# Kernel tuning notes

Hardware: AMD Instinct MI355X
Metric: run time of the kernel (lower is better)

## Reference

```python
import jax, jax.numpy as jnp
import numpy as np

N_NODES = 50000   # number of graph nodes
N_EDGES = 800000  # avg degree 16
D = 128           # in_dim == all hdims -> residual active every layer
L = 3             # len(cfg['hdims'])


def setup_inputs() -> dict:
    key = jax.random.key(0)
    ks = jax.random.split(key, 8)
    scale = 1.0 / np.sqrt(D)
    x = jax.random.normal(ks[0], (N_NODES, D), dtype=jnp.float32)
    edge_index = jax.random.randint(ks[1], (2, N_EDGES), 0, N_NODES, dtype=jnp.int32)
    in_fc_w = jax.random.normal(ks[2], (D, D), dtype=jnp.float32) * scale
    in_fc_b = jnp.zeros((D,), dtype=jnp.float32)
    # GraphConv per layer: lin_rel (with bias) applied to aggregated neighbors,
    # lin_root (no bias) applied to self features. All layers are DxD -> stack.
    w_rel = jax.random.normal(ks[3], (L, D, D), dtype=jnp.float32) * scale
    b_rel = jnp.zeros((L, D), dtype=jnp.float32)
    w_root = jax.random.normal(ks[4], (L, D, D), dtype=jnp.float32) * scale
    return {"x": x, "edge_index": edge_index, "in_fc_w": in_fc_w,
            "in_fc_b": in_fc_b, "w_rel": w_rel, "b_rel": b_rel, "w_root": w_root}


def reference(x, edge_index, in_fc_w, in_fc_b, w_rel, b_rel, w_root):
    src, dst = edge_index[0], edge_index[1]
    h = x @ in_fc_w + in_fc_b                     # in_fc
    for l in range(L):                            # fixed small layer count
        # GraphConv, aggr='add': gather source feats, scatter-add to targets
        agg = jax.ops.segment_sum(h[src], dst, num_segments=N_NODES)  # [N, D]
        out = agg @ w_rel[l] + b_rel[l] + h @ w_root[l]
        out = jax.nn.relu(out)
        h = out + h                               # residual (dims match)
    return h
```

## Files before the change

kernel.cpp:

```cpp
#include <hip/hip_runtime.h>
#include <hip/hip_bf16.h>


constexpr int D = 128;
constexpr int NB_SHIFT = 7;
constexpr int BCAP = 2560;
constexpr int STRIDE = 3456;
constexpr int CHUNK = 2048;
constexpr int NRANGE = 16;

typedef __attribute__((ext_vector_type(8))) short bf16x8;
typedef __attribute__((ext_vector_type(4))) float f32x4;
typedef __attribute__((ext_vector_type(4))) unsigned int u32x4;

__device__ inline unsigned short f2bf(float f) {
    unsigned int u = __builtin_bit_cast(unsigned int, f);
    u += 0x7FFFu + ((u >> 16) & 1u);
    return (unsigned short)(u >> 16);
}
__device__ inline float bf2f(unsigned short v) {
    return __builtin_bit_cast(float, (unsigned int)v << 16);
}
__device__ inline float bf2f_lo(unsigned int v) {
    return __builtin_bit_cast(float, v << 16);
}
__device__ inline float bf2f_hi(unsigned int v) {
    return __builtin_bit_cast(float, v & 0xFFFF0000u);
}

__global__ __launch_bounds__(256) void prep(
    const float* __restrict__ fc_w, const float* __restrict__ w_rel,
    const float* __restrict__ w_root, unsigned short* __restrict__ Wp,
    int* __restrict__ cursor, unsigned short* __restrict__ hb0,
    unsigned short* __restrict__ hb1, int NB, int N)
{
    int blk = blockIdx.x;
    if (blk < 56) {
        int idx = blk * 256 + threadIdx.x;
        int mat  = idx >> 11;
        int rem  = idx & 2047;
        int tn   = rem >> 8;
        int ks   = (rem >> 6) & 3;
        int lane = rem & 63;
        const float* w = (mat == 0) ? fc_w
                       : (mat <= 3) ? w_rel  + (size_t)(mat - 1) * D * D
                                    : w_root + (size_t)(mat - 4) * D * D;
        unsigned short* wp = Wp + (size_t)mat * D * D + (size_t)rem * 8;
        int kbase = ks * 32 + (lane >> 4) * 8;
        int col   = tn * 16 + (lane & 15);
        #pragma unroll
        for (int j = 0; j < 8; ++j)
            wp[j] = f2bf(w[(size_t)(kbase + j) * D + col]);
        return;
    }
    blk -= 56;
    const int ncb = (NB + 255) / 256;
    if (blk < ncb) {
        int i = blk * 256 + threadIdx.x;
        if (i < NB) cursor[i] = 0;
        return;
    }
    if (threadIdx.x < 64)
        ((unsigned int*)(hb0 + (size_t)N * D))[threadIdx.x] = 0u;
    else if (threadIdx.x < 128)
        ((unsigned int*)(hb1 + (size_t)N * D))[threadIdx.x - 64] = 0u;
}

__global__ __launch_bounds__(256) void scatter_gemm(
    const int* __restrict__ src, const int* __restrict__ dst,
    unsigned int* __restrict__ entries, int* __restrict__ cursor, int E, int NB, int NS,
    const float* __restrict__ x, const unsigned short* __restrict__ W1p,
    const float* __restrict__ bias, unsigned short* __restrict__ hb_out, int N)
{
    const int tid = threadIdx.x;

    if (blockIdx.x < (unsigned)NS) {
        __shared__ unsigned int   stage[CHUNK];
        __shared__ unsigned short bslot[CHUNK];
        __shared__ int lhist[512];
        __shared__ int lscan[512];
        __shared__ int lgbase[512];
        __shared__ int lcur[512];
        __shared__ int sh[256];

        const int base  = blockIdx.x * CHUNK;
        const int count = min(CHUNK, E - base);

        for (int i = tid; i < 512; i += 256) { lhist[i] = 0; lcur[i] = 0; }
        __syncthreads();

        for (int i = tid; i < count; i += 256)
            atomicAdd(&lhist[dst[base + i] >> NB_SHIFT], 1);
        __syncthreads();

        int v2 = lhist[2 * tid] + lhist[2 * tid + 1];
        sh[tid] = v2;
        __syncthreads();
        #pragma unroll
        for (int off = 1; off < 256; off <<= 1) {
            int t = (tid >= off) ? sh[tid - off] : 0;
            __syncthreads();
            sh[tid] += t;
            __syncthreads();
        }
        int excl2 = sh[tid] - v2;
        lscan[2 * tid]     = excl2;
        lscan[2 * tid + 1] = excl2 + lhist[2 * tid];
        __syncthreads();

        for (int t = tid; t < 512; t += 256) {
            int c = (t < NB) ? lhist[t] : 0;
            lgbase[t] = (c > 0) ? atomicAdd(&cursor[t], c) : 0;
        }
        __syncthreads();

        for (int i = tid; i < count; i += 256) {
            int d = dst[base + i];
            int s = src[base + i];
            int b = d >> NB_SHIFT;
            int p = atomicAdd(&lcur[b], 1);
            int slot = lscan[b] + p;
            stage[slot] = ((unsigned int)(d & ((1 << NB_SHIFT) - 1)) << 16) | (unsigned int)s;
            bslot[slot] = (unsigned short)b;
        }
        __syncthreads();

        for (int i = tid; i < count; i += 256) {
            int b   = bslot[i];
            int off = i - lscan[b] + lgbase[b];
            if (off < BCAP) entries[(size_t)b * BCAP + off] = stage[i];
        }
        return;
    }

    const int blk  = blockIdx.x - NS;
    const int wave = tid >> 6;
    const int lane = tid & 63;
    const int row0 = blk * 64 + wave * 16;
    const int mrow = lane & 15;
    const int kgrp = lane >> 4;

    f32x4 acc[8];
    #pragma unroll
    for (int t = 0; t < 8; ++t) acc[t] = (f32x4){0.f, 0.f, 0.f, 0.f};

    int arow = row0 + mrow; if (arow >= N) arow = N - 1;
    const float* xr = x + (size_t)arow * D + kgrp * 8;

    #pragma unroll
    for (int ks = 0; ks < 4; ++ks) {
        float4 f0 = *(const float4*)(xr + ks * 32);
        float4 f1 = *(const float4*)(xr + ks * 32 + 4);
        bf16x8 a1;
        a1[0] = (short)f2bf(f0.x); a1[1] = (short)f2bf(f0.y);
        a1[2] = (short)f2bf(f0.z); a1[3] = (short)f2bf(f0.w);
        a1[4] = (short)f2bf(f1.x); a1[5] = (short)f2bf(f1.y);
        a1[6] = (short)f2bf(f1.z); a1[7] = (short)f2bf(f1.w);
        #pragma unroll
        for (int tn = 0; tn < 8; ++tn) {
            bf16x8 b = *(const bf16x8*)(W1p + ((size_t)((tn * 4 + ks) * 64 + lane) * 8));
            acc[tn] = __builtin_amdgcn_mfma_f32_16x16x32_bf16(a1, b, acc[tn], 0, 0, 0);
        }
    }

    const int r0 = row0 + kgrp * 4;
    #pragma unroll
    for (int tn = 0; tn < 8; ++tn) {
        const int col = tn * 16 + mrow;
        const float bv = bias[col];
        #pragma unroll
        for (int reg = 0; reg < 4; ++reg) {
            int r = r0 + reg;
            if (r < N) hb_out[(size_t)r * D + col] = f2bf(acc[tn][reg] + bv);
        }
    }
}

__global__ __launch_bounds__(256) void bucket_sort(
    const unsigned int* __restrict__ entries, const int* __restrict__ cursor,
    unsigned int* __restrict__ sorted_off, int* __restrict__ eb,
    int N, int NB, float inv_range, unsigned int zero_off)
{
    const int b   = blockIdx.x;
    const int tid = threadIdx.x;

    __shared__ int nhist[128 * NRANGE];
    __shared__ int nscan[128 * NRANGE];
    __shared__ int ncur[128 * NRANGE];
    __shared__ int nbase[129];
    __shared__ int sh[256];
    __shared__ unsigned int svals[STRIDE];

    const int cnt = min(cursor[b], BCAP);

    for (int i = tid; i < 128 * NRANGE; i += 256) { nhist[i] = 0; ncur[i] = 0; }
    __syncthreads();

    const unsigned int* ebase = entries + (size_t)b * BCAP;
    for (int i = tid; i < cnt; i += 256) {
        unsigned int e = ebase[i];
        int s = (int)(e & 0xFFFFu);
        int r = (int)((float)s * inv_range); if (r > NRANGE - 1) r = NRANGE - 1;
        atomicAdd(&nhist[(int)((e >> 16) << 4) | r], 1);
    }
    __syncthreads();

    int c4 = 0, pc = 0;
    if (tid < 128) {
        int s = 0;
        #pragma unroll
        for (int q = 0; q < NRANGE; ++q) s += nhist[NRANGE * tid + q];
        c4 = s;
        pc = (c4 + 7) & ~7;
    }
    sh[tid] = (tid < 128) ? pc : 0;
    __syncthreads();
    #pragma unroll
    for (int off = 1; off < 128; off <<= 1) {
        int t = (tid >= off && tid < 128) ? sh[tid - off] : 0;
        __syncthreads();
        if (tid < 128) sh[tid] += t;
        __syncthreads();
    }
    if (tid < 128) nbase[tid] = sh[tid] - pc;
    if (tid == 127) nbase[128] = sh[127];
    __syncthreads();
    const int padded_total = nbase[128];

    if (tid < 128) {
        int base = nbase[tid];
        int run = base;
        #pragma unroll
        for (int q = 0; q < NRANGE; ++q) {
            nscan[NRANGE * tid + q] = run;
            run += nhist[NRANGE * tid + q];
        }
        int nn = (b << NB_SHIFT) + tid;
        if (nn < N) {
            eb[2 * nn]     = b * STRIDE + base;
            eb[2 * nn + 1] = b * STRIDE + base + pc;
        }
    }
    for (int i = tid; i < padded_total; i += 256) svals[i] = zero_off;
    __syncthreads();

    for (int i = tid; i < cnt; i += 256) {
        unsigned int e = ebase[i];
        int s = (int)(e & 0xFFFFu);
        int r = (int)((float)s * inv_range); if (r > NRANGE - 1) r = NRANGE - 1;
        int key = (int)((e >> 16) << 4) | r;
        int p = atomicAdd(&ncur[key], 1);
        svals[nscan[key] + p] = ((unsigned int)s) << 8;
    }
    __syncthreads();

    unsigned int* obase = sorted_off + (size_t)b * STRIDE;
    for (int i = tid; i < padded_total; i += 256) obase[i] = svals[i];
}

__global__ __launch_bounds__(256) void layer_fused(
    const unsigned short* __restrict__ hb_in, const int* __restrict__ eb,
    const unsigned int* __restrict__ sorted_off,
    const unsigned short* __restrict__ Wrel, const unsigned short* __restrict__ Wroot,
    const float* __restrict__ bias,
    unsigned short* hb_out, float* out_f32, int N)
{
    __shared__ unsigned short aggt[16][136];

    const int tid   = threadIdx.x;
    const int wave  = tid >> 6;
    const int lane  = tid & 63;
    const int node0 = blockIdx.x * 16;

    {
        const int g = lane >> 4;
        const int c = lane & 15;
        const int n = node0 + wave * 4 + g;

        float acc[8];
        #pragma unroll
        for (int q = 0; q < 8; ++q) acc[q] = 0.f;

        if (n < N) {
            const int2 be = ((const int2*)eb)[n];
            int j = be.x;
            const int e = be.y;
            const unsigned int c16 = (unsigned int)c * 16u;
            const char* hb = (const char*)hb_in;
            if (j < e) {
                u32x4 iA = *(const u32x4*)(sorted_off + j);
                u32x4 iB = *(const u32x4*)(sorted_off + j + 4);
                for (;;) {
                    u32x4 v0 = *(const u32x4*)(hb + (iA[0] + c16));
                    u32x4 v1 = *(const u32x4*)(hb + (iA[1] + c16));
                    u32x4 v2 = *(const u32x4*)(hb + (iA[2] + c16));
                    u32x4 v3 = *(const u32x4*)(hb + (iA[3] + c16));
                    u32x4 v4 = *(const u32x4*)(hb + (iB[0] + c16));
                    u32x4 v5 = *(const u32x4*)(hb + (iB[1] + c16));
                    u32x4 v6 = *(const u32x4*)(hb + (iB[2] + c16));
                    u32x4 v7 = *(const u32x4*)(hb + (iB[3] + c16));
                    const bool more = (j + 8 < e);
                    u32x4 nA, nB;
                    if (more) {
                        nA = *(const u32x4*)(sorted_off + j + 8);
                        nB = *(const u32x4*)(sorted_off + j + 12);
                    }
                    #pragma unroll
                    for (int q = 0; q < 4; ++q) {
                        acc[2 * q]     += ((bf2f_lo(v0[q]) + bf2f_lo(v1[q])) + (bf2f_lo(v2[q]) + bf2f_lo(v3[q])))
                                        + ((bf2f_lo(v4[q]) + bf2f_lo(v5[q])) + (bf2f_lo(v6[q]) + bf2f_lo(v7[q])));
                        acc[2 * q + 1] += ((bf2f_hi(v0[q]) + bf2f_hi(v1[q])) + (bf2f_hi(v2[q]) + bf2f_hi(v3[q])))
                                        + ((bf2f_hi(v4[q]) + bf2f_hi(v5[q])) + (bf2f_hi(v6[q]) + bf2f_hi(v7[q])));
                    }
                    if (!more) break;
                    iA = nA; iB = nB; j += 8;
                }
            }
        }
        u32x4 o;
        #pragma unroll
        for (int q = 0; q < 4; ++q)
            o[q] = (unsigned int)f2bf(acc[2 * q]) |
                   ((unsigned int)f2bf(acc[2 * q + 1]) << 16);
        *(u32x4*)&aggt[wave * 4 + g][c * 8] = o;
    }
    __syncthreads();

    const int mrow = lane & 15;
    const int kgrp = lane >> 4;

    f32x4 acc2[2];
    acc2[0] = (f32x4){0.f, 0.f, 0.f, 0.f};
    acc2[1] = (f32x4){0.f, 0.f, 0.f, 0.f};

    int arow = node0 + mrow; if (arow >= N) arow = N - 1;
    const size_t abase = (size_t)arow * D + kgrp * 8;

    #pragma unroll
    for (int ks = 0; ks < 4; ++ks) {
        bf16x8 a1 = *(const bf16x8*)&aggt[mrow][ks * 32 + kgrp * 8];
        bf16x8 a2 = *(const bf16x8*)(hb_in + abase + ks * 32);
        #pragma unroll
        for (int t = 0; t < 2; ++t) {
            const int tn = wave * 2 + t;
            bf16x8 b1 = *(const bf16x8*)(Wrel  + ((size_t)((tn * 4 + ks) * 64 + lane) * 8));
            acc2[t] = __builtin_amdgcn_mfma_f32_16x16x32_bf16(a1, b1, acc2[t], 0, 0, 0);
            bf16x8 b2 = *(const bf16x8*)(Wroot + ((size_t)((tn * 4 + ks) * 64 + lane) * 8));
            acc2[t] = __builtin_amdgcn_mfma_f32_16x16x32_bf16(a2, b2, acc2[t], 0, 0, 0);
        }
    }

    const int r0 = node0 + kgrp * 4;
    #pragma unroll
    for (int t = 0; t < 2; ++t) {
        const int tn  = wave * 2 + t;
        const int col = tn * 16 + mrow;
        const float bv = bias[col];
        #pragma unroll
        for (int reg = 0; reg < 4; ++reg) {
            int r = r0 + reg;
            if (r < N) {
                float z = fmaxf(acc2[t][reg] + bv, 0.f);
                float o = z + bf2f(hb_in[(size_t)r * D + col]);
                if (out_f32 != nullptr) out_f32[(size_t)r * D + col] = o;
                else                    hb_out[(size_t)r * D + col] = f2bf(o);
            }
        }
    }
}

extern "C" void kernel_launch(void* const* d_in, const int* in_sizes, int n_in,
                              void* d_out, int out_size, void* d_ws, size_t ws_size,
                              hipStream_t stream)
{
    const float* x      = (const float*)d_in[0];
    const int*   ei     = (const int*)  d_in[1];
    const float* fc_w   = (const float*)d_in[2];
    const float* fc_b   = (const float*)d_in[3];
    const float* w_rel  = (const float*)d_in[4];
    const float* b_rel  = (const float*)d_in[5];
    const float* w_root = (const float*)d_in[6];
    float* out = (float*)d_out;

    const int N = in_sizes[0] / D;
    const int E = in_sizes[1] / 2;
    const int* src = ei;
    const int* dst = ei + E;
    const int NB = (N + (1 << NB_SHIFT) - 1) >> NB_SHIFT;

    char* p = (char*)d_ws;
    unsigned short* hb0 = (unsigned short*)p;  p += (size_t)(N + 1) * D * sizeof(unsigned short);
    unsigned short* hb1 = (unsigned short*)p;  p += (size_t)(N + 1) * D * sizeof(unsigned short);
    unsigned short* Wp  = (unsigned short*)p;  p += (size_t)7 * D * D * sizeof(unsigned short);
    unsigned int* sorted_off = (unsigned int*)p;  p += (size_t)NB * STRIDE * sizeof(unsigned int);
    int* eb     = (int*)p;                     p += (size_t)2 * N * sizeof(int);
    int* cursor = (int*)p;                     p += (size_t)NB * sizeof(int);
    unsigned int* entries = (unsigned int*)d_out;

    unsigned short* Wp_in   = Wp;
    unsigned short* Wp_rel  = Wp + (size_t)1 * D * D;
    unsigned short* Wp_root = Wp + (size_t)4 * D * D;

    const int NS = (E + CHUNK - 1) / CHUNK;
    const int gemm_blocks  = (N + 63) / 64;
    const int layer_blocks = (N + 15) / 16;
    const int prep_blocks  = 56 + (NB + 255) / 256 + 1;

    prep<<<prep_blocks, 256, 0, stream>>>(fc_w, w_rel, w_root, Wp, cursor,
                                          hb0, hb1, NB, N);

    scatter_gemm<<<NS + gemm_blocks, 256, 0, stream>>>(
        src, dst, entries, cursor, E, NB, NS,
        x, Wp_in, fc_b, hb0, N);

    bucket_sort<<<NB, 256, 0, stream>>>(
        entries, cursor, sorted_off, eb, N, NB, (float)NRANGE / (float)N,
        ((unsigned int)N) << 8);

    unsigned short* hin  = hb0;
    unsigned short* hout = hb1;
    for (int l = 0; l < 3; ++l) {
        layer_fused<<<layer_blocks, 256, 0, stream>>>(
            hin, eb, sorted_off,
            Wp_rel + (size_t)l * D * D, Wp_root + (size_t)l * D * D,
            b_rel + (size_t)l * D,
            (l == 2) ? nullptr : hout,
            (l == 2) ? out : nullptr, N);
        unsigned short* t = hin; hin = hout; hout = t;
    }
}
```

Measured before the change: 229.5 us.

## Split node features into column chunks and separate gather from GEMM

Stores the bf16 node features as four column chunks of 32 features each, so a gather block only touches a 3.2 MB slice that fits in cache better. Each layer is split into a chunk-parallel gather kernel that writes the aggregate to global memory, plus a separate GEMM/epilogue kernel. Sorted source indices are compressed from 32-bit byte offsets to 16-bit node ids. This adds an extra round trip through global memory for the aggregate and one more launch per layer. The 16-bit ids only hold while N is below 65536.

New measurement: 247.5 us. 1.08x slower.

```diff
diff --git a/kernel.cpp b/kernel.cpp
--- a/kernel.cpp
+++ b/kernel.cpp
@@ -32,7 +32,7 @@
     const float* __restrict__ fc_w, const float* __restrict__ w_rel,
     const float* __restrict__ w_root, unsigned short* __restrict__ Wp,
     int* __restrict__ cursor, unsigned short* __restrict__ hb0,
-    unsigned short* __restrict__ hb1, int NB, int N)
+    unsigned short* __restrict__ hb1, int NB, int N, int CSr)
 {
     int blk = blockIdx.x;
     if (blk < 56) {
@@ -60,17 +60,22 @@
         if (i < NB) cursor[i] = 0;
         return;
     }
-    if (threadIdx.x < 64)
-        ((unsigned int*)(hb0 + (size_t)N * D))[threadIdx.x] = 0u;
-    else if (threadIdx.x < 128)
-        ((unsigned int*)(hb1 + (size_t)N * D))[threadIdx.x - 64] = 0u;
+    const int t = threadIdx.x;
+    if (t < 64) {
+        int c = t >> 4, w = t & 15;
+        ((unsigned int*)(hb0 + (size_t)c * CSr + (size_t)N * 32))[w] = 0u;
+    } else if (t < 128) {
+        int tt = t - 64;
+        int c = tt >> 4, w = tt & 15;
+        ((unsigned int*)(hb1 + (size_t)c * CSr + (size_t)N * 32))[w] = 0u;
+    }
 }
 
 __global__ __launch_bounds__(256) void scatter_gemm(
     const int* __restrict__ src, const int* __restrict__ dst,
     unsigned int* __restrict__ entries, int* __restrict__ cursor, int E, int NB, int NS,
     const float* __restrict__ x, const unsigned short* __restrict__ W1p,
-    const float* __restrict__ bias, unsigned short* __restrict__ hb_out, int N)
+    const float* __restrict__ bias, unsigned short* __restrict__ hb_out, int N, int CSr)
 {
     const int tid = threadIdx.x;
 
@@ -168,18 +173,21 @@
     for (int tn = 0; tn < 8; ++tn) {
         const int col = tn * 16 + mrow;
         const float bv = bias[col];
+        const int c  = col >> 5;
+        const int cc = col & 31;
         #pragma unroll
         for (int reg = 0; reg < 4; ++reg) {
             int r = r0 + reg;
-            if (r < N) hb_out[(size_t)r * D + col] = f2bf(acc[tn][reg] + bv);
+            if (r < N)
+                hb_out[(size_t)c * CSr + (size_t)r * 32 + cc] = f2bf(acc[tn][reg] + bv);
         }
     }
 }
 
 __global__ __launch_bounds__(256) void bucket_sort(
     const unsigned int* __restrict__ entries, const int* __restrict__ cursor,
-    unsigned int* __restrict__ sorted_off, int* __restrict__ eb,
-    int N, int NB, float inv_range, unsigned int zero_off)
+    unsigned short* __restrict__ sorted_src, int* __restrict__ eb,
+    int N, int NB, float inv_range, int zero_id)
 {
     const int b   = blockIdx.x;
     const int tid = threadIdx.x;
@@ -189,7 +197,7 @@
     __shared__ int ncur[128 * NRANGE];
     __shared__ int nbase[129];
     __shared__ int sh[256];
-    __shared__ unsigned int svals[STRIDE];
+    __shared__ unsigned short svals[STRIDE];
 
     const int cnt = min(cursor[b], BCAP);
 
@@ -241,7 +249,7 @@
             eb[2 * nn + 1] = b * STRIDE + base + pc;
         }
     }
-    for (int i = tid; i < padded_total; i += 256) svals[i] = zero_off;
+    for (int i = tid; i < padded_total; i += 256) svals[i] = (unsigned short)zero_id;
     __syncthreads();
 
     for (int i = tid; i < cnt; i += 256) {
@@ -250,71 +258,66 @@
         int r = (int)((float)s * inv_range); if (r > NRANGE - 1) r = NRANGE - 1;
         int key = (int)((e >> 16) << 4) | r;
         int p = atomicAdd(&ncur[key], 1);
-        svals[nscan[key] + p] = ((unsigned int)s) << 8;
-    }
-    __syncthreads();
-
-    unsigned int* obase = sorted_off + (size_t)b * STRIDE;
+        svals[nscan[key] + p] = (unsigned short)s;
+    }
+    __syncthreads();
+
+    unsigned short* obase = sorted_src + (size_t)b * STRIDE;
     for (int i = tid; i < padded_total; i += 256) obase[i] = svals[i];
 }
 
-__global__ __launch_bounds__(256) void layer_fused(
+__global__ __launch_bounds__(256) void gather8(
     const unsigned short* __restrict__ hb_in, const int* __restrict__ eb,
-    const unsigned int* __restrict__ sorted_off,
-    const unsigned short* __restrict__ Wrel, const unsigned short* __restrict__ Wroot,
-    const float* __restrict__ bias,
-    unsigned short* hb_out, float* out_f32, int N)
-{
-    __shared__ unsigned short aggt[16][136];
-
+    const unsigned short* __restrict__ sorted_src,
+    unsigned short* __restrict__ aggb, int N, int CSr)
+{
     const int tid   = threadIdx.x;
+    const int chunk = blockIdx.x & 3;
+    const int tile  = blockIdx.x >> 2;
+    const int lane  = tid & 63;
     const int wave  = tid >> 6;
-    const int lane  = tid & 63;
-    const int node0 = blockIdx.x * 16;
-
-    {
-        const int g = lane >> 4;
-        const int c = lane & 15;
-        const int n = node0 + wave * 4 + g;
-
-        float acc[8];
-        #pragma unroll
-        for (int q = 0; q < 8; ++q) acc[q] = 0.f;
-
-        if (n < N) {
-            const int2 be = ((const int2*)eb)[n];
-            int j = be.x;
-            const int e = be.y;
-            const unsigned int c16 = (unsigned int)c * 16u;
-            const char* hb = (const char*)hb_in;
-            if (j < e) {
-                u32x4 iA = *(const u32x4*)(sorted_off + j);
-                u32x4 iB = *(const u32x4*)(sorted_off + j + 4);
-                for (;;) {
-                    u32x4 v0 = *(const u32x4*)(hb + (iA[0] + c16));
-                    u32x4 v1 = *(const u32x4*)(hb + (iA[1] + c16));
-                    u32x4 v2 = *(const u32x4*)(hb + (iA[2] + c16));
-                    u32x4 v3 = *(const u32x4*)(hb + (iA[3] + c16));
-                    u32x4 v4 = *(const u32x4*)(hb + (iB[0] + c16));
-                    u32x4 v5 = *(const u32x4*)(hb + (iB[1] + c16));
-                    u32x4 v6 = *(const u32x4*)(hb + (iB[2] + c16));
-                    u32x4 v7 = *(const u32x4*)(hb + (iB[3] + c16));
-                    const bool more = (j + 8 < e);
-                    u32x4 nA, nB;
-                    if (more) {
-                        nA = *(const u32x4*)(sorted_off + j + 8);
-                        nB = *(const u32x4*)(sorted_off + j + 12);
-                    }
-                    #pragma unroll
-                    for (int q = 0; q < 4; ++q) {
-                        acc[2 * q]     += ((bf2f_lo(v0[q]) + bf2f_lo(v1[q])) + (bf2f_lo(v2[q]) + bf2f_lo(v3[q])))
-                                        + ((bf2f_lo(v4[q]) + bf2f_lo(v5[q])) + (bf2f_lo(v6[q]) + bf2f_lo(v7[q])));
-                        acc[2 * q + 1] += ((bf2f_hi(v0[q]) + bf2f_hi(v1[q])) + (bf2f_hi(v2[q]) + bf2f_hi(v3[q])))
-                                        + ((bf2f_hi(v4[q]) + bf2f_hi(v5[q])) + (bf2f_hi(v6[q]) + bf2f_hi(v7[q])));
-                    }
-                    if (!more) break;
-                    iA = nA; iB = nB; j += 8;
+    const int g     = lane >> 2;
+    const int sub   = lane & 3;
+    const int n     = tile * 64 + wave * 16 + g;
+
+    const unsigned short* hbc = hb_in + (size_t)chunk * CSr;
+    const unsigned int sub8 = (unsigned int)sub * 8;
+
+    float acc[8];
+    #pragma unroll
+    for (int q = 0; q < 8; ++q) acc[q] = 0.f;
+
+    if (n < N) {
+        const int2 be = ((const int2*)eb)[n];
+        int j = be.x;
+        const int e = be.y;
+        if (j < e) {
+            u32x4 I = *(const u32x4*)(sorted_src + j);
+            for (;;) {
+                unsigned int s0 = I[0] & 0xFFFFu, s1 = I[0] >> 16;
+                unsigned int s2 = I[1] & 0xFFFFu, s3 = I[1] >> 16;
+                unsigned int s4 = I[2] & 0xFFFFu, s5 = I[2] >> 16;
+                unsigned int s6 = I[3] & 0xFFFFu, s7 = I[3] >> 16;
+                u32x4 v0 = *(const u32x4*)(hbc + (size_t)s0 * 32 + sub8);
+                u32x4 v1 = *(const u32x4*)(hbc + (size_t)s1 * 32 + sub8);
+                u32x4 v2 = *(const u32x4*)(hbc + (size_t)s2 * 32 + sub8);
+                u32x4 v3 = *(const u32x4*)(hbc + (size_t)s3 * 32 + sub8);
+                u32x4 v4 = *(const u32x4*)(hbc + (size_t)s4 * 32 + sub8);
+                u32x4 v5 = *(const u32x4*)(hbc + (size_t)s5 * 32 + sub8);
+                u32x4 v6 = *(const u32x4*)(hbc + (size_t)s6 * 32 + sub8);
+                u32x4 v7 = *(const u32x4*)(hbc + (size_t)s7 * 32 + sub8);
+                const bool more = (j + 8 < e);
+                u32x4 nI;
+                if (more) nI = *(const u32x4*)(sorted_src + j + 8);
+                #pragma unroll
+                for (int q = 0; q < 4; ++q) {
+                    acc[2 * q]     += ((bf2f_lo(v0[q]) + bf2f_lo(v1[q])) + (bf2f_lo(v2[q]) + bf2f_lo(v3[q])))
+                                    + ((bf2f_lo(v4[q]) + bf2f_lo(v5[q])) + (bf2f_lo(v6[q]) + bf2f_lo(v7[q])));
+                    acc[2 * q + 1] += ((bf2f_hi(v0[q]) + bf2f_hi(v1[q])) + (bf2f_hi(v2[q]) + bf2f_hi(v3[q])))
+                                    + ((bf2f_hi(v4[q]) + bf2f_hi(v5[q])) + (bf2f_hi(v6[q]) + bf2f_hi(v7[q])));
                 }
+                if (!more) break;
+                I = nI; j += 8;
             }
         }
         u32x4 o;
@@ -322,48 +325,58 @@
         for (int q = 0; q < 4; ++q)
             o[q] = (unsigned int)f2bf(acc[2 * q]) |
                    ((unsigned int)f2bf(acc[2 * q + 1]) << 16);
-        *(u32x4*)&aggt[wave * 4 + g][c * 8] = o;
-    }
-    __syncthreads();
-
+        *(u32x4*)(aggb + (size_t)n * D + chunk * 32 + sub8) = o;
+    }
+}
+
+__global__ __launch_bounds__(256) void gemm_epi(
+    const unsigned short* __restrict__ aggb, const unsigned short* __restrict__ hb_in,
+    const unsigned short* __restrict__ Wrel, const unsigned short* __restrict__ Wroot,
+    const float* __restrict__ bias, unsigned short* hb_out, float* out_f32,
+    int N, int CSr)
+{
+    const int tid  = threadIdx.x;
+    const int wave = tid >> 6;
+    const int lane = tid & 63;
+    const int row0 = blockIdx.x * 64 + wave * 16;
     const int mrow = lane & 15;
     const int kgrp = lane >> 4;
 
-    f32x4 acc2[2];
-    acc2[0] = (f32x4){0.f, 0.f, 0.f, 0.f};
-    acc2[1] = (f32x4){0.f, 0.f, 0.f, 0.f};
-
-    int arow = node0 + mrow; if (arow >= N) arow = N - 1;
-    const size_t abase = (size_t)arow * D + kgrp * 8;
+    f32x4 acc[8];
+    #pragma unroll
+    for (int t = 0; t < 8; ++t) acc[t] = (f32x4){0.f, 0.f, 0.f, 0.f};
+
+    int arow = row0 + mrow; if (arow >= N) arow = N - 1;
+    const unsigned short* ag = aggb + (size_t)arow * D + kgrp * 8;
 
     #pragma unroll
     for (int ks = 0; ks < 4; ++ks) {
-        bf16x8 a1 = *(const bf16x8*)&aggt[mrow][ks * 32 + kgrp * 8];
-        bf16x8 a2 = *(const bf16x8*)(hb_in + abase + ks * 32);
-        #pragma unroll
-        for (int t = 0; t < 2; ++t) {
-            const int tn = wave * 2 + t;
+        bf16x8 a1 = *(const bf16x8*)(ag + ks * 32);
+        bf16x8 a2 = *(const bf16x8*)(hb_in + (size_t)ks * CSr + (size_t)arow * 32 + kgrp * 8);
+        #pragma unroll
+        for (int tn = 0; tn < 8; ++tn) {
             bf16x8 b1 = *(const bf16x8*)(Wrel  + ((size_t)((tn * 4 + ks) * 64 + lane) * 8));
-            acc2[t] = __builtin_amdgcn_mfma_f32_16x16x32_bf16(a1, b1, acc2[t], 0, 0, 0);
+            acc[tn] = __builtin_amdgcn_mfma_f32_16x16x32_bf16(a1, b1, acc[tn], 0, 0, 0);
             bf16x8 b2 = *(const bf16x8*)(Wroot + ((size_t)((tn * 4 + ks) * 64 + lane) * 8));
-            acc2[t] = __builtin_amdgcn_mfma_f32_16x16x32_bf16(a2, b2, acc2[t], 0, 0, 0);
-        }
-    }
-
-    const int r0 = node0 + kgrp * 4;
-    #pragma unroll
-    for (int t = 0; t < 2; ++t) {
-        const int tn  = wave * 2 + t;
+            acc[tn] = __builtin_amdgcn_mfma_f32_16x16x32_bf16(a2, b2, acc[tn], 0, 0, 0);
+        }
+    }
+
+    const int r0 = row0 + kgrp * 4;
+    #pragma unroll
+    for (int tn = 0; tn < 8; ++tn) {
         const int col = tn * 16 + mrow;
         const float bv = bias[col];
+        const int c  = col >> 5;
+        const int cc = col & 31;
         #pragma unroll
         for (int reg = 0; reg < 4; ++reg) {
             int r = r0 + reg;
             if (r < N) {
-                float z = fmaxf(acc2[t][reg] + bv, 0.f);
-                float o = z + bf2f(hb_in[(size_t)r * D + col]);
+                float z = fmaxf(acc[tn][reg] + bv, 0.f);
+                float o = z + bf2f(hb_in[(size_t)c * CSr + (size_t)r * 32 + cc]);
                 if (out_f32 != nullptr) out_f32[(size_t)r * D + col] = o;
-                else                    hb_out[(size_t)r * D + col] = f2bf(o);
+                else hb_out[(size_t)c * CSr + (size_t)r * 32 + cc] = f2bf(o);
             }
         }
     }
@@ -387,14 +400,16 @@
     const int* src = ei;
     const int* dst = ei + E;
     const int NB = (N + (1 << NB_SHIFT) - 1) >> NB_SHIFT;
+    const int CSr = (N + 1) * 32;
 
     char* p = (char*)d_ws;
-    unsigned short* hb0 = (unsigned short*)p;  p += (size_t)(N + 1) * D * sizeof(unsigned short);
-    unsigned short* hb1 = (unsigned short*)p;  p += (size_t)(N + 1) * D * sizeof(unsigned short);
-    unsigned short* Wp  = (unsigned short*)p;  p += (size_t)7 * D * D * sizeof(unsigned short);
-    unsigned int* sorted_off = (unsigned int*)p;  p += (size_t)NB * STRIDE * sizeof(unsigned int);
-    int* eb     = (int*)p;                     p += (size_t)2 * N * sizeof(int);
-    int* cursor = (int*)p;                     p += (size_t)NB * sizeof(int);
+    unsigned short* hb0  = (unsigned short*)p;  p += (size_t)4 * CSr * sizeof(unsigned short);
+    unsigned short* hb1  = (unsigned short*)p;  p += (size_t)4 * CSr * sizeof(unsigned short);
+    unsigned short* aggb = (unsigned short*)p;  p += (size_t)N * D * sizeof(unsigned short);
+    unsigned short* Wp   = (unsigned short*)p;  p += (size_t)7 * D * D * sizeof(unsigned short);
+    unsigned short* sorted_src = (unsigned short*)p;  p += (size_t)NB * STRIDE * sizeof(unsigned short);
+    int* eb     = (int*)p;                      p += (size_t)2 * N * sizeof(int);
+    int* cursor = (int*)p;                      p += (size_t)NB * sizeof(int);
     unsigned int* entries = (unsigned int*)d_out;
 
     unsigned short* Wp_in   = Wp;
@@ -402,30 +417,30 @@
     unsigned short* Wp_root = Wp + (size_t)4 * D * D;
 
     const int NS = (E + CHUNK - 1) / CHUNK;
-    const int gemm_blocks  = (N + 63) / 64;
-    const int layer_blocks = (N + 15) / 16;
-    const int prep_blocks  = 56 + (NB + 255) / 256 + 1;
+    const int gemm_blocks   = (N + 63) / 64;
+    const int tiles         = (N + 63) / 64;
+    const int prep_blocks   = 56 + (NB + 255) / 256 + 1;
 
     prep<<<prep_blocks, 256, 0, stream>>>(fc_w, w_rel, w_root, Wp, cursor,
-                                          hb0, hb1, NB, N);
+                                          hb0, hb1, NB, N, CSr);
 
     scatter_gemm<<<NS + gemm_blocks, 256, 0, stream>>>(
         src, dst, entries, cursor, E, NB, NS,
-        x, Wp_in, fc_b, hb0, N);
+        x, Wp_in, fc_b, hb0, N, CSr);
 
     bucket_sort<<<NB, 256, 0, stream>>>(
-        entries, cursor, sorted_off, eb, N, NB, (float)NRANGE / (float)N,
-        ((unsigned int)N) << 8);
+        entries, cursor, sorted_src, eb, N, NB, (float)NRANGE / (float)N, N);
 
     unsigned short* hin  = hb0;
     unsigned short* hout = hb1;
     for (int l = 0; l < 3; ++l) {
-        layer_fused<<<layer_blocks, 256, 0, stream>>>(
-            hin, eb, sorted_off,
+        gather8<<<tiles * 4, 256, 0, stream>>>(hin, eb, sorted_src, aggb, N, CSr);
+        gemm_epi<<<gemm_blocks, 256, 0, stream>>>(
+            aggb, hin,
             Wp_rel + (size_t)l * D * D, Wp_root + (size_t)l * D * D,
             b_rel + (size_t)l * D,
             (l == 2) ? nullptr : hout,
-            (l == 2) ? out : nullptr, N);
+            (l == 2) ? out : nullptr, N, CSr);
         unsigned short* t = hin; hin = hout; hout = t;
     }
 }
```

## Compute per-node degree during scatter and drop source-range subsorting in bucket sort

Applied to the files above, without the earlier changes.

Adds per-node degree counting via global atomics in the scatter pass, so bucket_sort no longer needs its own histogram pass over the entries. It also drops the 16-way source-range sub-bucketing, which previously ordered each node's neighbors by source index for gather locality. This removes one pass over the entries and shrinks shared memory in bucket_sort. In exchange it adds 800k global atomics to scatter, and the layer gathers lose source-locality ordering.

Result: slower. 252.4 us (+10.0%).

```diff
diff --git a/kernel.cpp b/kernel.cpp
--- a/kernel.cpp
+++ b/kernel.cpp
@@ -7,7 +7,6 @@
 constexpr int BCAP = 2560;
 constexpr int STRIDE = 3456;
 constexpr int CHUNK = 2048;
-constexpr int NRANGE = 16;
 
 typedef __attribute__((ext_vector_type(8))) short bf16x8;
 typedef __attribute__((ext_vector_type(4))) float f32x4;
@@ -31,8 +30,9 @@
 __global__ __launch_bounds__(256) void prep(
     const float* __restrict__ fc_w, const float* __restrict__ w_rel,
     const float* __restrict__ w_root, unsigned short* __restrict__ Wp,
-    int* __restrict__ cursor, unsigned short* __restrict__ hb0,
-    unsigned short* __restrict__ hb1, int NB, int N)
+    int* __restrict__ cursor, int* __restrict__ deg,
+    unsigned short* __restrict__ hb0, unsigned short* __restrict__ hb1,
+    int NB, int N)
 {
     int blk = blockIdx.x;
     if (blk < 56) {
@@ -60,6 +60,13 @@
         if (i < NB) cursor[i] = 0;
         return;
     }
+    blk -= ncb;
+    const int ndb = (N + 255) / 256;
+    if (blk < ndb) {
+        int i = blk * 256 + threadIdx.x;
+        if (i < N) deg[i] = 0;
+        return;
+    }
     if (threadIdx.x < 64)
         ((unsigned int*)(hb0 + (size_t)N * D))[threadIdx.x] = 0u;
     else if (threadIdx.x < 128)
@@ -68,7 +75,8 @@
 
 __global__ __launch_bounds__(256) void scatter_gemm(
     const int* __restrict__ src, const int* __restrict__ dst,
-    unsigned int* __restrict__ entries, int* __restrict__ cursor, int E, int NB, int NS,
+    unsigned int* __restrict__ entries, int* __restrict__ cursor,
+    int* __restrict__ deg, int E, int NB, int NS,
     const float* __restrict__ x, const unsigned short* __restrict__ W1p,
     const float* __restrict__ bias, unsigned short* __restrict__ hb_out, int N)
 {
@@ -89,8 +97,11 @@
         for (int i = tid; i < 512; i += 256) { lhist[i] = 0; lcur[i] = 0; }
         __syncthreads();
 
-        for (int i = tid; i < count; i += 256)
-            atomicAdd(&lhist[dst[base + i] >> NB_SHIFT], 1);
+        for (int i = tid; i < count; i += 256) {
+            int dd = dst[base + i];
+            atomicAdd(&lhist[dd >> NB_SHIFT], 1);
+            atomicAdd(&deg[dd], 1);
+        }
         __syncthreads();
 
         int v2 = lhist[2 * tid] + lhist[2 * tid + 1];
@@ -178,42 +189,28 @@
 
 __global__ __launch_bounds__(256) void bucket_sort(
     const unsigned int* __restrict__ entries, const int* __restrict__ cursor,
+    const int* __restrict__ deg,
     unsigned int* __restrict__ sorted_off, int* __restrict__ eb,
-    int N, int NB, float inv_range, unsigned int zero_off)
+    int N, int NB, unsigned int zero_off)
 {
     const int b   = blockIdx.x;
     const int tid = threadIdx.x;
 
-    __shared__ int nhist[128 * NRANGE];
-    __shared__ int nscan[128 * NRANGE];
-    __shared__ int ncur[128 * NRANGE];
-    __shared__ int nbase[129];
-    __shared__ int sh[256];
+    __shared__ int nscan[129];
+    __shared__ int ncur[128];
+    __shared__ int sh[128];
     __shared__ unsigned int svals[STRIDE];
 
     const int cnt = min(cursor[b], BCAP);
 
-    for (int i = tid; i < 128 * NRANGE; i += 256) { nhist[i] = 0; ncur[i] = 0; }
-    __syncthreads();
-
-    const unsigned int* ebase = entries + (size_t)b * BCAP;
-    for (int i = tid; i < cnt; i += 256) {
-        unsigned int e = ebase[i];
-        int s = (int)(e & 0xFFFFu);
-        int r = (int)((float)s * inv_range); if (r > NRANGE - 1) r = NRANGE - 1;
-        atomicAdd(&nhist[(int)((e >> 16) << 4) | r], 1);
-    }
-    __syncthreads();
-
-    int c4 = 0, pc = 0;
+    int d = 0, pc = 0;
     if (tid < 128) {
-        int s = 0;
-        #pragma unroll
-        for (int q = 0; q < NRANGE; ++q) s += nhist[NRANGE * tid + q];
-        c4 = s;
-        pc = (c4 + 7) & ~7;
-    }
-    sh[tid] = (tid < 128) ? pc : 0;
+        int nn = (b << NB_SHIFT) + tid;
+        d  = (nn < N) ? deg[nn] : 0;
+        pc = (d + 7) & ~7;
+        ncur[tid] = 0;
+        sh[tid]   = pc;
+    }
     __syncthreads();
     #pragma unroll
     for (int off = 1; off < 128; off <<= 1) {
@@ -222,35 +219,28 @@
         if (tid < 128) sh[tid] += t;
         __syncthreads();
     }
-    if (tid < 128) nbase[tid] = sh[tid] - pc;
-    if (tid == 127) nbase[128] = sh[127];
-    __syncthreads();
-    const int padded_total = nbase[128];
-
     if (tid < 128) {
-        int base = nbase[tid];
-        int run = base;
-        #pragma unroll
-        for (int q = 0; q < NRANGE; ++q) {
-            nscan[NRANGE * tid + q] = run;
-            run += nhist[NRANGE * tid + q];
-        }
+        int base = sh[tid] - pc;
+        nscan[tid] = base;
         int nn = (b << NB_SHIFT) + tid;
         if (nn < N) {
             eb[2 * nn]     = b * STRIDE + base;
             eb[2 * nn + 1] = b * STRIDE + base + pc;
         }
     }
+    if (tid == 127) nscan[128] = sh[127];
+    __syncthreads();
+    const int padded_total = nscan[128];
+
     for (int i = tid; i < padded_total; i += 256) svals[i] = zero_off;
     __syncthreads();
 
+    const unsigned int* ebase = entries + (size_t)b * BCAP;
     for (int i = tid; i < cnt; i += 256) {
-        unsigned int e = ebase[i];
-        int s = (int)(e & 0xFFFFu);
-        int r = (int)((float)s * inv_range); if (r > NRANGE - 1) r = NRANGE - 1;
-        int key = (int)((e >> 16) << 4) | r;
-        int p = atomicAdd(&ncur[key], 1);
-        svals[nscan[key] + p] = ((unsigned int)s) << 8;
+        unsigned int e  = ebase[i];
+        int dl = (int)(e >> 16);
+        int p  = atomicAdd(&ncur[dl], 1);
+        svals[nscan[dl] + p] = (e & 0xFFFFu) << 8;
     }
     __syncthreads();
 
@@ -395,6 +385,7 @@
     unsigned int* sorted_off = (unsigned int*)p;  p += (size_t)NB * STRIDE * sizeof(unsigned int);
     int* eb     = (int*)p;                     p += (size_t)2 * N * sizeof(int);
     int* cursor = (int*)p;                     p += (size_t)NB * sizeof(int);
+    int* deg    = (int*)p;                     p += (size_t)N * sizeof(int);
     unsigned int* entries = (unsigned int*)d_out;
 
     unsigned short* Wp_in   = Wp;
@@ -404,17 +395,17 @@
     const int NS = (E + CHUNK - 1) / CHUNK;
     const int gemm_blocks  = (N + 63) / 64;
     const int layer_blocks = (N + 15) / 16;
-    const int prep_blocks  = 56 + (NB + 255) / 256 + 1;
-
-    prep<<<prep_blocks, 256, 0, stream>>>(fc_w, w_rel, w_root, Wp, cursor,
+    const int prep_blocks  = 56 + (NB + 255) / 256 + (N + 255) / 256 + 1;
+
+    prep<<<prep_blocks, 256, 0, stream>>>(fc_w, w_rel, w_root, Wp, cursor, deg,
                                           hb0, hb1, NB, N);
 
     scatter_gemm<<<NS + gemm_blocks, 256, 0, stream>>>(
-        src, dst, entries, cursor, E, NB, NS,
+        src, dst, entries, cursor, deg, E, NB, NS,
         x, Wp_in, fc_b, hb0, N);
 
     bucket_sort<<<NB, 256, 0, stream>>>(
-        entries, cursor, sorted_off, eb, N, NB, (float)NRANGE / (float)N,
+        entries, cursor, deg, sorted_off, eb, N, NB,
         ((unsigned int)N) << 8);
 
     unsigned short* hin  = hb0;
```
